# Kernel tuning notes

Hardware: AMD Instinct MI355X
Metric: run time of the kernel (lower is better)

The kernel has to match this reference:

```python
import jax, jax.numpy as jnp
import numpy as np

N, E, IN, H, C = 20000, 320000, 512, 4, 64
HC = H * C
EPS_BN = 1e-5


def setup_inputs() -> dict:
    key = jax.random.key(0)
    ks = jax.random.split(key, 12)
    p = lambda k, shape, s=0.05: jax.random.normal(k, shape, dtype=jnp.float32) * s
    z = lambda n: jnp.zeros((n,), jnp.float32)
    o = lambda n: jnp.ones((n,), jnp.float32)
    return {
        "x": jax.random.normal(ks[0], (N, IN), dtype=jnp.float32),
        "edge_index": jax.random.randint(ks[1], (2, E), 0, N),
        "Wl0": p(ks[2], (IN, HC)), "Wr0": p(ks[3], (IN, HC)),
        "att0": p(ks[4], (H, C)), "b0": z(HC),
        "g0": o(HC), "be0": z(HC), "m0": z(HC), "v0": o(HC),
        "Wl1": p(ks[5], (HC, HC)), "Wr1": p(ks[6], (HC, HC)),
        "att1": p(ks[7], (H, C)), "b1": z(HC),
        "g1": o(HC), "be1": z(HC), "m1": z(HC), "v1": o(HC),
        "Wl2": p(ks[8], (HC, 2)), "Wr2": p(ks[9], (HC, 2)),
        "att2": p(ks[10], (1, 2)), "b2": z(2),
    }


def gatv2_conv(x, Wl, Wr, att, b, ei, concat):
    # GATv2: e_ij = att . LeakyReLU(Wl x_j + Wr x_i); softmax over in-edges of i
    n = x.shape[0]
    h, c = att.shape
    xl = (x @ Wl).reshape(n, h, c)  # source/message transform
    xr = (x @ Wr).reshape(n, h, c)  # target transform
    src, dst = ei[0], ei[1]
    m = xl[src] + xr[dst]                                   # [E,H,C] edge gather
    e = jnp.sum(jax.nn.leaky_relu(m, 0.2) * att, axis=-1)   # [E,H]
    emax = jax.ops.segment_max(e, dst, num_segments=n)      # segment softmax
    emax = jnp.where(jnp.isfinite(emax), emax, 0.0)
    ex = jnp.exp(e - emax[dst])
    denom = jax.ops.segment_sum(ex, dst, num_segments=n)
    alpha = ex / (denom[dst] + 1e-16)                       # [E,H]
    out = jax.ops.segment_sum(alpha[:, :, None] * xl[src], dst, num_segments=n)
    out = out.reshape(n, h * c) if concat else out.mean(axis=1)
    return out + b


def bn_eval(x, g, be, m, v):
    return (x - m) * (g * jax.lax.rsqrt(v + EPS_BN)) + be


def reference(x, edge_index, Wl0, Wr0, att0, b0, g0, be0, m0, v0,
              Wl1, Wr1, att1, b1, g1, be1, m1, v1, Wl2, Wr2, att2, b2):
    loops = jnp.arange(N)
    ei = jnp.concatenate([edge_index, jnp.stack([loops, loops])], axis=1)
    h = gatv2_conv(x, Wl0, Wr0, att0, b0, ei, True)
    h = jax.nn.elu(bn_eval(h, g0, be0, m0, v0))
    h = gatv2_conv(h, Wl1, Wr1, att1, b1, ei, True)
    h = jax.nn.elu(bn_eval(h, g1, be1, m1, v1))
    out = gatv2_conv(h, Wl2, Wr2, att2, b2, ei, False)
    return jax.nn.log_softmax(out, axis=1)
```

## Files before the change

kernel.cpp:

```cpp
#include <hip/hip_runtime.h>
#include <math.h>

#define NN 20000
#define MP 20096
#define EE 320000
#define ET (EE + NN)
#define HC 256
#define EPS_BN 1e-5f

typedef __bf16 bf16x8 __attribute__((ext_vector_type(8)));
typedef float f32x4 __attribute__((ext_vector_type(4)));

__device__ __forceinline__ float4 ld4(const float* p) { return *reinterpret_cast<const float4*>(p); }
__device__ __forceinline__ float lrelu(float x) { return fmaxf(x, 0.f) + 0.2f * fminf(x, 0.f); }

__device__ __forceinline__ unsigned short f2b(float f) {
  unsigned int u = __float_as_uint(f);
  u = (u + 0x7fffu + ((u >> 16) & 1u)) >> 16;
  return (unsigned short)u;
}
__device__ __forceinline__ float b2f(unsigned short u) {
  return __uint_as_float(((unsigned int)u) << 16);
}

__device__ __forceinline__ void gld_lds16(const void* g, void* l) {
  __builtin_amdgcn_global_load_lds(
      (const __attribute__((address_space(1))) unsigned int*)g,
      (__attribute__((address_space(3))) unsigned int*)(unsigned int)(unsigned long long)l,
      16, 0, 0);
}

__global__ __launch_bounds__(256) void convert_x_kernel(const float* __restrict__ x,
                                                        unsigned short* __restrict__ xb) {
  int i = (blockIdx.x * 256 + threadIdx.x) * 4;
  if (i >= NN * 512) return;
  float4 v = ld4(&x[i]);
  ushort4 o;
  o.x = f2b(v.x); o.y = f2b(v.y); o.z = f2b(v.z); o.w = f2b(v.w);
  *reinterpret_cast<ushort4*>(&xb[i]) = o;
}

__global__ __launch_bounds__(256) void convert_w_kernel(const float* __restrict__ Wl,
                                                        const float* __restrict__ Wr,
                                                        unsigned short* __restrict__ Wf,
                                                        int K) {
  int idx = blockIdx.x * 256 + threadIdx.x;
  if (idx >= 512 * K) return;
  int n = idx / K, k = idx - n * K;
  float v = (n < 256) ? Wl[(size_t)k * 256 + n] : Wr[(size_t)k * 256 + (n - 256)];
  Wf[idx] = f2b(v);
}

__global__ __launch_bounds__(256) void gemm_mfma(const unsigned short* __restrict__ A,
                                                 const unsigned short* __restrict__ Bt,
                                                 unsigned short* __restrict__ xlb,
                                                 float* __restrict__ xrf,
                                                 int M, int K) {
  __shared__ unsigned short As[128 * 32];
  __shared__ unsigned short Bs[128 * 32];
  const int wave = threadIdx.x >> 6;
  const int lane = threadIdx.x & 63;
  const int am = lane & 15;
  const int aq = lane >> 4;
  const int wr = (wave >> 1) * 64;
  const int wc = (wave & 1) * 64;
  const int row0 = blockIdx.y * 128;
  const int col0 = blockIdx.x * 128;

  f32x4 acc[4][4] = {};

  for (int kk = 0; kk < K; kk += 32) {
    __syncthreads();
#pragma unroll
    for (int c = 0; c < 2; ++c) {
      int seg = wave * 128 + c * 64 + lane;
      int r = seg >> 2, ks = (seg & 3) * 8;
      gld_lds16(A + (size_t)(row0 + r) * K + kk + ks, &As[(wave * 128 + c * 64) * 8]);
      gld_lds16(Bt + (size_t)(col0 + r) * K + kk + ks, &Bs[(wave * 128 + c * 64) * 8]);
    }
    __syncthreads();

    bf16x8 af[4], bfr[4];
#pragma unroll
    for (int i = 0; i < 4; ++i)
      af[i] = *reinterpret_cast<const bf16x8*>(&As[(wr + i * 16 + am) * 32 + aq * 8]);
#pragma unroll
    for (int j = 0; j < 4; ++j)
      bfr[j] = *reinterpret_cast<const bf16x8*>(&Bs[(wc + j * 16 + am) * 32 + aq * 8]);
#pragma unroll
    for (int i = 0; i < 4; ++i)
#pragma unroll
      for (int j = 0; j < 4; ++j)
        acc[i][j] = __builtin_amdgcn_mfma_f32_16x16x32_bf16(af[i], bfr[j], acc[i][j], 0, 0, 0);
  }

#pragma unroll
  for (int i = 0; i < 4; ++i) {
#pragma unroll
    for (int j = 0; j < 4; ++j) {
      int gcol = col0 + wc + j * 16 + am;
#pragma unroll
      for (int rr = 0; rr < 4; ++rr) {
        int grow = row0 + wr + i * 16 + aq * 4 + rr;
        if (grow < M) {
          float v = acc[i][j][rr];
          if (gcol < 256) xlb[(size_t)grow * 256 + gcol] = f2b(v);
          else            xrf[(size_t)grow * 256 + (gcol - 256)] = v;
        }
      }
    }
  }
}

__global__ __launch_bounds__(256) void hist_kernel(const int* __restrict__ ei,
                                                   int* __restrict__ counts) {
  int e = blockIdx.x * blockDim.x + threadIdx.x;
  if (e >= ET) return;
  int d = (e < EE) ? ei[EE + e] : (e - EE);
  atomicAdd(&counts[d], 1);
}

__global__ __launch_bounds__(1024) void scan_kernel(int* __restrict__ cursor,
                                                    int* __restrict__ offsets) {
  __shared__ int wsum[16];
  const int tid = threadIdx.x;
  const int lane = tid & 63, wv = tid >> 6;
  const int base = tid * 20;
  int vals[20];
  int s = 0;
  if (tid < 1000) {
#pragma unroll
    for (int j = 0; j < 20; ++j) { vals[j] = cursor[base + j]; s += vals[j]; }
  }
  int ssum = s;
#pragma unroll
  for (int off = 1; off < 64; off <<= 1) {
    int t = __shfl_up(ssum, off);
    if (lane >= off) ssum += t;
  }
  if (lane == 63) wsum[wv] = ssum;
  __syncthreads();
  if (wv == 0) {
    int w = (lane < 16) ? wsum[lane] : 0;
#pragma unroll
    for (int off = 1; off < 16; off <<= 1) {
      int t = __shfl_up(w, off);
      if (lane >= off) w += t;
    }
    if (lane < 16) wsum[lane] = w;
  }
  __syncthreads();
  int excl = ssum - s + (wv > 0 ? wsum[wv - 1] : 0);
  if (tid < 1000) {
    int run = excl;
#pragma unroll
    for (int j = 0; j < 20; ++j) { offsets[base + j] = run; cursor[base + j] = run; run += vals[j]; }
  }
  if (tid == 1023) offsets[NN] = wsum[15];
}

__global__ __launch_bounds__(256) void scatter_kernel(const int* __restrict__ ei,
                                                      int* __restrict__ cursor,
                                                      int* __restrict__ srcs) {
  int e = blockIdx.x * blockDim.x + threadIdx.x;
  if (e >= ET) return;
  int s, d;
  if (e < EE) { s = ei[e]; d = ei[EE + e]; } else { s = d = e - EE; }
  int pos = atomicAdd(&cursor[d], 1);
  srcs[pos] = s;
}

__global__ __launch_bounds__(256) void gat_layer(const unsigned short* __restrict__ xlb,
                                                 const float* __restrict__ xrf,
                                                 const float* __restrict__ att,
                                                 const float* __restrict__ bias,
                                                 const float* __restrict__ gam,
                                                 const float* __restrict__ bet,
                                                 const float* __restrict__ mean,
                                                 const float* __restrict__ var,
                                                 const int* __restrict__ offsets,
                                                 const int* __restrict__ srcs,
                                                 unsigned short* __restrict__ hb) {
  const int wave = threadIdx.x >> 6;
  const int lane = threadIdx.x & 63;
  const int node = blockIdx.x * 4 + wave;
  if (node >= NN) return;

  const float4 xr4 = ld4(&xrf[(size_t)node * HC + lane * 4]);
  const float4 a4 = ld4(&att[lane * 4]);
  const int beg = offsets[node];
  const int end = offsets[node + 1];

  float lA = 0.f, lB = 0.f;
  float4 OA = make_float4(0.f, 0.f, 0.f, 0.f);
  float4 OB = make_float4(0.f, 0.f, 0.f, 0.f);

  int i = beg;
  for (; i + 3 < end; i += 4) {
    int s0 = srcs[i], s1 = srcs[i + 1], s2 = srcs[i + 2], s3 = srcs[i + 3];
    ushort4 u0 = *reinterpret_cast<const ushort4*>(&xlb[(size_t)s0 * HC + lane * 4]);
    ushort4 u1 = *reinterpret_cast<const ushort4*>(&xlb[(size_t)s1 * HC + lane * 4]);
    ushort4 u2 = *reinterpret_cast<const ushort4*>(&xlb[(size_t)s2 * HC + lane * 4]);
    ushort4 u3 = *reinterpret_cast<const ushort4*>(&xlb[(size_t)s3 * HC + lane * 4]);
    float4 x0 = make_float4(b2f(u0.x), b2f(u0.y), b2f(u0.z), b2f(u0.w));
    float4 x1 = make_float4(b2f(u1.x), b2f(u1.y), b2f(u1.z), b2f(u1.w));
    float4 x2 = make_float4(b2f(u2.x), b2f(u2.y), b2f(u2.z), b2f(u2.w));
    float4 x3 = make_float4(b2f(u3.x), b2f(u3.y), b2f(u3.z), b2f(u3.w));
    float e0 = lrelu(x0.x + xr4.x) * a4.x + lrelu(x0.y + xr4.y) * a4.y +
               lrelu(x0.z + xr4.z) * a4.z + lrelu(x0.w + xr4.w) * a4.w;
    float e1 = lrelu(x1.x + xr4.x) * a4.x + lrelu(x1.y + xr4.y) * a4.y +
               lrelu(x1.z + xr4.z) * a4.z + lrelu(x1.w + xr4.w) * a4.w;
    float e2 = lrelu(x2.x + xr4.x) * a4.x + lrelu(x2.y + xr4.y) * a4.y +
               lrelu(x2.z + xr4.z) * a4.z + lrelu(x2.w + xr4.w) * a4.w;
    float e3 = lrelu(x3.x + xr4.x) * a4.x + lrelu(x3.y + xr4.y) * a4.y +
               lrelu(x3.z + xr4.z) * a4.z + lrelu(x3.w + xr4.w) * a4.w;
#pragma unroll
    for (int off = 1; off < 16; off <<= 1) {
      e0 += __shfl_xor(e0, off);
      e1 += __shfl_xor(e1, off);
      e2 += __shfl_xor(e2, off);
      e3 += __shfl_xor(e3, off);
    }
    float p0 = __expf(e0), p1 = __expf(e1), p2 = __expf(e2), p3 = __expf(e3);
    lA += p0; lB += p1; lA += p2; lB += p3;
    OA.x += p0 * x0.x; OA.y += p0 * x0.y; OA.z += p0 * x0.z; OA.w += p0 * x0.w;
    OB.x += p1 * x1.x; OB.y += p1 * x1.y; OB.z += p1 * x1.z; OB.w += p1 * x1.w;
    OA.x += p2 * x2.x; OA.y += p2 * x2.y; OA.z += p2 * x2.z; OA.w += p2 * x2.w;
    OB.x += p3 * x3.x; OB.y += p3 * x3.y; OB.z += p3 * x3.z; OB.w += p3 * x3.w;
  }
  for (; i < end; ++i) {
    int s = srcs[i];
    ushort4 u = *reinterpret_cast<const ushort4*>(&xlb[(size_t)s * HC + lane * 4]);
    float4 x0 = make_float4(b2f(u.x), b2f(u.y), b2f(u.z), b2f(u.w));
    float e = lrelu(x0.x + xr4.x) * a4.x + lrelu(x0.y + xr4.y) * a4.y +
              lrelu(x0.z + xr4.z) * a4.z + lrelu(x0.w + xr4.w) * a4.w;
#pragma unroll
    for (int off = 1; off < 16; off <<= 1) e += __shfl_xor(e, off);
    float p = __expf(e);
    lA += p;
    OA.x += p * x0.x; OA.y += p * x0.y; OA.z += p * x0.z; OA.w += p * x0.w;
  }
  float inv = 1.f / (lA + lB);
  float4 O = make_float4(OA.x + OB.x, OA.y + OB.y, OA.z + OB.z, OA.w + OB.w);

  float4 b4 = ld4(&bias[lane * 4]);
  float4 g4 = ld4(&gam[lane * 4]);
  float4 e4 = ld4(&bet[lane * 4]);
  float4 m4 = ld4(&mean[lane * 4]);
  float4 v4 = ld4(&var[lane * 4]);
  float y0 = O.x * inv + b4.x, y1 = O.y * inv + b4.y;
  float y2 = O.z * inv + b4.z, y3 = O.w * inv + b4.w;
  float z0 = (y0 - m4.x) * (g4.x * rsqrtf(v4.x + EPS_BN)) + e4.x;
  float z1 = (y1 - m4.y) * (g4.y * rsqrtf(v4.y + EPS_BN)) + e4.y;
  float z2 = (y2 - m4.z) * (g4.z * rsqrtf(v4.z + EPS_BN)) + e4.z;
  float z3 = (y3 - m4.w) * (g4.w * rsqrtf(v4.w + EPS_BN)) + e4.w;
  ushort4 r;
  r.x = f2b(z0 > 0.f ? z0 : expm1f(z0));
  r.y = f2b(z1 > 0.f ? z1 : expm1f(z1));
  r.z = f2b(z2 > 0.f ? z2 : expm1f(z2));
  r.w = f2b(z3 > 0.f ? z3 : expm1f(z3));
  *reinterpret_cast<ushort4*>(&hb[(size_t)node * HC + lane * 4]) = r;
}

__global__ __launch_bounds__(256) void lin2_kernel(const unsigned short* __restrict__ hb,
                                                   const float* __restrict__ Wl,
                                                   const float* __restrict__ Wr,
                                                   float* __restrict__ xl2,
                                                   float* __restrict__ xr2) {
  const int wave = threadIdx.x >> 6;
  const int lane = threadIdx.x & 63;
  const int node = blockIdx.x * 4 + wave;
  if (node >= NN) return;
  ushort4 h4 = *reinterpret_cast<const ushort4*>(&hb[(size_t)node * HC + lane * 4]);
  float hv[4] = {b2f(h4.x), b2f(h4.y), b2f(h4.z), b2f(h4.w)};
  float l0 = 0.f, l1 = 0.f, r0 = 0.f, r1 = 0.f;
#pragma unroll
  for (int j = 0; j < 4; ++j) {
    int row = lane * 4 + j;
    l0 += hv[j] * Wl[row * 2 + 0];
    l1 += hv[j] * Wl[row * 2 + 1];
    r0 += hv[j] * Wr[row * 2 + 0];
    r1 += hv[j] * Wr[row * 2 + 1];
  }
#pragma unroll
  for (int off = 1; off < 64; off <<= 1) {
    l0 += __shfl_xor(l0, off);
    l1 += __shfl_xor(l1, off);
    r0 += __shfl_xor(r0, off);
    r1 += __shfl_xor(r1, off);
  }
  if (lane == 0) {
    xl2[node * 2 + 0] = l0; xl2[node * 2 + 1] = l1;
    xr2[node * 2 + 0] = r0; xr2[node * 2 + 1] = r1;
  }
}

__global__ __launch_bounds__(256) void gat2_out_kernel(const float* __restrict__ xl2,
                                                       const float* __restrict__ xr2,
                                                       const float* __restrict__ att2,
                                                       const float* __restrict__ b2,
                                                       const int* __restrict__ offsets,
                                                       const int* __restrict__ srcs,
                                                       float* __restrict__ out) {
  const int wave = threadIdx.x >> 6;
  const int lane = threadIdx.x & 63;
  const int node = blockIdx.x * 4 + wave;
  if (node >= NN) return;
  const float a0 = att2[0], a1 = att2[1];
  const float xr0 = xr2[node * 2 + 0], xr1 = xr2[node * 2 + 1];
  const int beg = offsets[node], end = offsets[node + 1];

  float l = 0.f, o0 = 0.f, o1 = 0.f;
  for (int i = beg + lane; i < end; i += 64) {
    int s = srcs[i];
    float x0 = xl2[s * 2 + 0], x1 = xl2[s * 2 + 1];
    float e = lrelu(x0 + xr0) * a0 + lrelu(x1 + xr1) * a1;
    float p = __expf(e);
    l += p;
    o0 += p * x0;
    o1 += p * x1;
  }
#pragma unroll
  for (int off = 1; off < 64; off <<= 1) {
    l += __shfl_xor(l, off);
    o0 += __shfl_xor(o0, off);
    o1 += __shfl_xor(o1, off);
  }
  if (lane == 0) {
    float inv = 1.f / l;
    float t0 = o0 * inv + b2[0];
    float t1 = o1 * inv + b2[1];
    float mx = fmaxf(t0, t1);
    float ls = mx + logf(__expf(t0 - mx) + __expf(t1 - mx));
    out[node * 2 + 0] = t0 - ls;
    out[node * 2 + 1] = t1 - ls;
  }
}

extern "C" void kernel_launch(void* const* d_in, const int* in_sizes, int n_in,
                              void* d_out, int out_size, void* d_ws, size_t ws_size,
                              hipStream_t stream) {
  const float* x    = (const float*)d_in[0];
  const int*   ei   = (const int*)d_in[1];
  const float* Wl0  = (const float*)d_in[2];
  const float* Wr0  = (const float*)d_in[3];
  const float* att0 = (const float*)d_in[4];
  const float* b0   = (const float*)d_in[5];
  const float* g0   = (const float*)d_in[6];
  const float* be0  = (const float*)d_in[7];
  const float* m0   = (const float*)d_in[8];
  const float* v0   = (const float*)d_in[9];
  const float* Wl1  = (const float*)d_in[10];
  const float* Wr1  = (const float*)d_in[11];
  const float* att1 = (const float*)d_in[12];
  const float* b1   = (const float*)d_in[13];
  const float* g1   = (const float*)d_in[14];
  const float* be1  = (const float*)d_in[15];
  const float* m1   = (const float*)d_in[16];
  const float* v1   = (const float*)d_in[17];
  const float* Wl2  = (const float*)d_in[18];
  const float* Wr2  = (const float*)d_in[19];
  const float* att2 = (const float*)d_in[20];
  const float* b2   = (const float*)d_in[21];

  float* xrf = (float*)d_ws;
  unsigned short* xlb = (unsigned short*)(xrf + (size_t)NN * 256);
  unsigned short* hb  = xlb + (size_t)NN * 256;
  unsigned short* xb  = hb + (size_t)MP * 256;
  unsigned short* Wf0 = xb + (size_t)MP * 512;
  unsigned short* Wf1 = Wf0 + 512 * 512;
  float* xl2 = (float*)(Wf1 + 512 * 256);
  float* xr2 = xl2 + 2 * NN;
  int* offsets = (int*)(xr2 + 2 * NN);
  int* cursor  = offsets + (NN + 1);
  int* srcs    = cursor + NN;

  hipMemsetAsync(cursor, 0, NN * sizeof(int), stream);
  hist_kernel<<<(ET + 255) / 256, 256, 0, stream>>>(ei, cursor);
  convert_x_kernel<<<(NN * 512 / 4 + 255) / 256, 256, 0, stream>>>(x, xb);
  convert_w_kernel<<<(512 * 512 + 255) / 256, 256, 0, stream>>>(Wl0, Wr0, Wf0, 512);
  convert_w_kernel<<<(512 * 256 + 255) / 256, 256, 0, stream>>>(Wl1, Wr1, Wf1, 256);
  scan_kernel<<<1, 1024, 0, stream>>>(cursor, offsets);
  scatter_kernel<<<(ET + 255) / 256, 256, 0, stream>>>(ei, cursor, srcs);

  dim3 gemm_grid(4, MP / 128);
  gemm_mfma<<<gemm_grid, 256, 0, stream>>>(xb, Wf0, xlb, xrf, NN, 512);
  gat_layer<<<NN / 4, 256, 0, stream>>>(xlb, xrf, att0, b0, g0, be0, m0, v0, offsets, srcs, hb);
  gemm_mfma<<<gemm_grid, 256, 0, stream>>>(hb, Wf1, xlb, xrf, NN, 256);
  gat_layer<<<NN / 4, 256, 0, stream>>>(xlb, xrf, att1, b1, g1, be1, m1, v1, offsets, srcs, hb);
  lin2_kernel<<<NN / 4, 256, 0, stream>>>(hb, Wl2, Wr2, xl2, xr2);
  gat2_out_kernel<<<NN / 4, 256, 0, stream>>>(xl2, xr2, att2, b2, offsets, srcs, (float*)d_out);
}
```

Baseline: 301.6 us.

## Fuse prep kernels and software-pipeline edge gathers in GAT layer

Merges the x conversion, both weight conversions and the degree histogram into one launch, split by block-index ranges, which removes three kernel launches and lets the pieces overlap. The GAT layer edge loop now loads up to 64 source indices per wave at once, hands them out with shuffles, and keeps three batches of 4-edge feature gathers in flight in a rotating buffer. This is meant to hide gather latency. In exchange it needs more registers and does extra masked work on partial batches.

```diff
diff --git a/kernel.cpp b/kernel.cpp
--- a/kernel.cpp
+++ b/kernel.cpp
@@ -8,6 +8,12 @@
 #define HC 256
 #define EPS_BN 1e-5f
 
+#define PB_CX 5000
+#define PB_W0 1024
+#define PB_W1 512
+#define PB_HIST 1329
+#define PB_TOTAL (PB_CX + PB_W0 + PB_W1 + PB_HIST)
+
 typedef __bf16 bf16x8 __attribute__((ext_vector_type(8)));
 typedef float f32x4 __attribute__((ext_vector_type(4)));
 
@@ -30,25 +36,44 @@
       16, 0, 0);
 }
 
-__global__ __launch_bounds__(256) void convert_x_kernel(const float* __restrict__ x,
-                                                        unsigned short* __restrict__ xb) {
-  int i = (blockIdx.x * 256 + threadIdx.x) * 4;
-  if (i >= NN * 512) return;
-  float4 v = ld4(&x[i]);
-  ushort4 o;
-  o.x = f2b(v.x); o.y = f2b(v.y); o.z = f2b(v.z); o.w = f2b(v.w);
-  *reinterpret_cast<ushort4*>(&xb[i]) = o;
-}
-
-__global__ __launch_bounds__(256) void convert_w_kernel(const float* __restrict__ Wl,
-                                                        const float* __restrict__ Wr,
-                                                        unsigned short* __restrict__ Wf,
-                                                        int K) {
-  int idx = blockIdx.x * 256 + threadIdx.x;
-  if (idx >= 512 * K) return;
-  int n = idx / K, k = idx - n * K;
-  float v = (n < 256) ? Wl[(size_t)k * 256 + n] : Wr[(size_t)k * 256 + (n - 256)];
-  Wf[idx] = f2b(v);
+__global__ __launch_bounds__(256) void prep_kernel(const float* __restrict__ x,
+                                                   unsigned short* __restrict__ xb,
+                                                   const float* __restrict__ Wl0,
+                                                   const float* __restrict__ Wr0,
+                                                   unsigned short* __restrict__ Wf0,
+                                                   const float* __restrict__ Wl1,
+                                                   const float* __restrict__ Wr1,
+                                                   unsigned short* __restrict__ Wf1,
+                                                   const int* __restrict__ ei,
+                                                   int* __restrict__ counts) {
+  const int b = blockIdx.x;
+  const int tid = threadIdx.x;
+  if (b < PB_CX) {
+    int i = (b * 256 + tid) * 8;
+    float4 v0 = ld4(&x[i]);
+    float4 v1 = ld4(&x[i + 4]);
+    ushort4 o0, o1;
+    o0.x = f2b(v0.x); o0.y = f2b(v0.y); o0.z = f2b(v0.z); o0.w = f2b(v0.w);
+    o1.x = f2b(v1.x); o1.y = f2b(v1.y); o1.z = f2b(v1.z); o1.w = f2b(v1.w);
+    *reinterpret_cast<ushort4*>(&xb[i]) = o0;
+    *reinterpret_cast<ushort4*>(&xb[i + 4]) = o1;
+  } else if (b < PB_CX + PB_W0) {
+    int idx = (b - PB_CX) * 256 + tid;
+    int n = idx >> 9, k = idx & 511;
+    float v = (n < 256) ? Wl0[(size_t)k * 256 + n] : Wr0[(size_t)k * 256 + (n - 256)];
+    Wf0[idx] = f2b(v);
+  } else if (b < PB_CX + PB_W0 + PB_W1) {
+    int idx = (b - PB_CX - PB_W0) * 256 + tid;
+    int n = idx >> 8, k = idx & 255;
+    float v = (n < 256) ? Wl1[(size_t)k * 256 + n] : Wr1[(size_t)k * 256 + (n - 256)];
+    Wf1[idx] = f2b(v);
+  } else {
+    int e = (b - PB_CX - PB_W0 - PB_W1) * 256 + tid;
+    if (e < ET) {
+      int d = (e < EE) ? ei[EE + e] : (e - EE);
+      atomicAdd(&counts[d], 1);
+    }
+  }
 }
 
 __global__ __launch_bounds__(256) void gemm_mfma(const unsigned short* __restrict__ A,
@@ -112,14 +137,6 @@
   }
 }
 
-__global__ __launch_bounds__(256) void hist_kernel(const int* __restrict__ ei,
-                                                   int* __restrict__ counts) {
-  int e = blockIdx.x * blockDim.x + threadIdx.x;
-  if (e >= ET) return;
-  int d = (e < EE) ? ei[EE + e] : (e - EE);
-  atomicAdd(&counts[d], 1);
-}
-
 __global__ __launch_bounds__(1024) void scan_kernel(int* __restrict__ cursor,
                                                     int* __restrict__ offsets) {
   __shared__ int wsum[16];
@@ -189,57 +206,76 @@
   const float4 xr4 = ld4(&xrf[(size_t)node * HC + lane * 4]);
   const float4 a4 = ld4(&att[lane * 4]);
   const int beg = offsets[node];
-  const int end = offsets[node + 1];
+  const int deg = offsets[node + 1] - beg;
 
   float lA = 0.f, lB = 0.f;
   float4 OA = make_float4(0.f, 0.f, 0.f, 0.f);
   float4 OB = make_float4(0.f, 0.f, 0.f, 0.f);
 
-  int i = beg;
-  for (; i + 3 < end; i += 4) {
-    int s0 = srcs[i], s1 = srcs[i + 1], s2 = srcs[i + 2], s3 = srcs[i + 3];
-    ushort4 u0 = *reinterpret_cast<const ushort4*>(&xlb[(size_t)s0 * HC + lane * 4]);
-    ushort4 u1 = *reinterpret_cast<const ushort4*>(&xlb[(size_t)s1 * HC + lane * 4]);
-    ushort4 u2 = *reinterpret_cast<const ushort4*>(&xlb[(size_t)s2 * HC + lane * 4]);
-    ushort4 u3 = *reinterpret_cast<const ushort4*>(&xlb[(size_t)s3 * HC + lane * 4]);
-    float4 x0 = make_float4(b2f(u0.x), b2f(u0.y), b2f(u0.z), b2f(u0.w));
-    float4 x1 = make_float4(b2f(u1.x), b2f(u1.y), b2f(u1.z), b2f(u1.w));
-    float4 x2 = make_float4(b2f(u2.x), b2f(u2.y), b2f(u2.z), b2f(u2.w));
-    float4 x3 = make_float4(b2f(u3.x), b2f(u3.y), b2f(u3.z), b2f(u3.w));
-    float e0 = lrelu(x0.x + xr4.x) * a4.x + lrelu(x0.y + xr4.y) * a4.y +
-               lrelu(x0.z + xr4.z) * a4.z + lrelu(x0.w + xr4.w) * a4.w;
-    float e1 = lrelu(x1.x + xr4.x) * a4.x + lrelu(x1.y + xr4.y) * a4.y +
-               lrelu(x1.z + xr4.z) * a4.z + lrelu(x1.w + xr4.w) * a4.w;
-    float e2 = lrelu(x2.x + xr4.x) * a4.x + lrelu(x2.y + xr4.y) * a4.y +
-               lrelu(x2.z + xr4.z) * a4.z + lrelu(x2.w + xr4.w) * a4.w;
-    float e3 = lrelu(x3.x + xr4.x) * a4.x + lrelu(x3.y + xr4.y) * a4.y +
-               lrelu(x3.z + xr4.z) * a4.z + lrelu(x3.w + xr4.w) * a4.w;
-#pragma unroll
-    for (int off = 1; off < 16; off <<= 1) {
-      e0 += __shfl_xor(e0, off);
-      e1 += __shfl_xor(e1, off);
-      e2 += __shfl_xor(e2, off);
-      e3 += __shfl_xor(e3, off);
-    }
-    float p0 = __expf(e0), p1 = __expf(e1), p2 = __expf(e2), p3 = __expf(e3);
-    lA += p0; lB += p1; lA += p2; lB += p3;
-    OA.x += p0 * x0.x; OA.y += p0 * x0.y; OA.z += p0 * x0.z; OA.w += p0 * x0.w;
-    OB.x += p1 * x1.x; OB.y += p1 * x1.y; OB.z += p1 * x1.z; OB.w += p1 * x1.w;
-    OA.x += p2 * x2.x; OA.y += p2 * x2.y; OA.z += p2 * x2.z; OA.w += p2 * x2.w;
-    OB.x += p3 * x3.x; OB.y += p3 * x3.y; OB.z += p3 * x3.z; OB.w += p3 * x3.w;
-  }
-  for (; i < end; ++i) {
-    int s = srcs[i];
-    ushort4 u = *reinterpret_cast<const ushort4*>(&xlb[(size_t)s * HC + lane * 4]);
-    float4 x0 = make_float4(b2f(u.x), b2f(u.y), b2f(u.z), b2f(u.w));
-    float e = lrelu(x0.x + xr4.x) * a4.x + lrelu(x0.y + xr4.y) * a4.y +
-              lrelu(x0.z + xr4.z) * a4.z + lrelu(x0.w + xr4.w) * a4.w;
-#pragma unroll
-    for (int off = 1; off < 16; off <<= 1) e += __shfl_xor(e, off);
-    float p = __expf(e);
-    lA += p;
-    OA.x += p * x0.x; OA.y += p * x0.y; OA.z += p * x0.z; OA.w += p * x0.w;
-  }
+  for (int base = 0; base < deg; base += 64) {
+    const int chunk = min(64, deg - base);
+    const int s_reg = srcs[beg + base + min(lane, chunk - 1)];
+    const int nb = (chunk + 3) >> 2;
+
+    ushort4 buf0[4], buf1[4], buf2[4];
+
+#define ISSUE(r, buf)                                                              \
+    {                                                                              \
+      _Pragma("unroll")                                                            \
+      for (int j = 0; j < 4; ++j) {                                                \
+        int idx = (r) * 4 + j;                                                     \
+        int sv = __shfl(s_reg, idx < chunk ? idx : 0);                             \
+        buf[j] = *reinterpret_cast<const ushort4*>(&xlb[(size_t)sv * HC + lane * 4]); \
+      }                                                                            \
+    }
+
+#define COMPUTE(r, buf)                                                            \
+    {                                                                              \
+      float e[4], xv[4][4];                                                        \
+      _Pragma("unroll")                                                            \
+      for (int j = 0; j < 4; ++j) {                                                \
+        xv[j][0] = b2f(buf[j].x); xv[j][1] = b2f(buf[j].y);                        \
+        xv[j][2] = b2f(buf[j].z); xv[j][3] = b2f(buf[j].w);                        \
+        e[j] = lrelu(xv[j][0] + xr4.x) * a4.x + lrelu(xv[j][1] + xr4.y) * a4.y +   \
+               lrelu(xv[j][2] + xr4.z) * a4.z + lrelu(xv[j][3] + xr4.w) * a4.w;    \
+      }                                                                            \
+      _Pragma("unroll")                                                            \
+      for (int off = 1; off < 16; off <<= 1) {                                     \
+        e[0] += __shfl_xor(e[0], off); e[1] += __shfl_xor(e[1], off);              \
+        e[2] += __shfl_xor(e[2], off); e[3] += __shfl_xor(e[3], off);              \
+      }                                                                            \
+      float p0 = __expf(e[0]), p1 = __expf(e[1]);                                  \
+      float p2 = __expf(e[2]), p3 = __expf(e[3]);                                  \
+      if ((r) * 4 + 0 >= chunk) p0 = 0.f;                                          \
+      if ((r) * 4 + 1 >= chunk) p1 = 0.f;                                          \
+      if ((r) * 4 + 2 >= chunk) p2 = 0.f;                                          \
+      if ((r) * 4 + 3 >= chunk) p3 = 0.f;                                          \
+      lA += p0; lB += p1; lA += p2; lB += p3;                                      \
+      OA.x += p0 * xv[0][0]; OA.y += p0 * xv[0][1];                                \
+      OA.z += p0 * xv[0][2]; OA.w += p0 * xv[0][3];                                \
+      OB.x += p1 * xv[1][0]; OB.y += p1 * xv[1][1];                                \
+      OB.z += p1 * xv[1][2]; OB.w += p1 * xv[1][3];                                \
+      OA.x += p2 * xv[2][0]; OA.y += p2 * xv[2][1];                                \
+      OA.z += p2 * xv[2][2]; OA.w += p2 * xv[2][3];                                \
+      OB.x += p3 * xv[3][0]; OB.y += p3 * xv[3][1];                                \
+      OB.z += p3 * xv[3][2]; OB.w += p3 * xv[3][3];                                \
+    }
+
+    ISSUE(0, buf0);
+    ISSUE(1, buf1);
+    ISSUE(2, buf2);
+    int r = 0;
+    while (r < nb) {
+      COMPUTE(r, buf0); if (r + 3 < nb) ISSUE(r + 3, buf0); ++r;
+      if (r >= nb) break;
+      COMPUTE(r, buf1); if (r + 3 < nb) ISSUE(r + 3, buf1); ++r;
+      if (r >= nb) break;
+      COMPUTE(r, buf2); if (r + 3 < nb) ISSUE(r + 3, buf2); ++r;
+    }
+#undef ISSUE
+#undef COMPUTE
+  }
+
   float inv = 1.f / (lA + lB);
   float4 O = make_float4(OA.x + OB.x, OA.y + OB.y, OA.z + OB.z, OA.w + OB.w);
 
@@ -254,12 +290,12 @@
   float z1 = (y1 - m4.y) * (g4.y * rsqrtf(v4.y + EPS_BN)) + e4.y;
   float z2 = (y2 - m4.z) * (g4.z * rsqrtf(v4.z + EPS_BN)) + e4.z;
   float z3 = (y3 - m4.w) * (g4.w * rsqrtf(v4.w + EPS_BN)) + e4.w;
-  ushort4 r;
-  r.x = f2b(z0 > 0.f ? z0 : expm1f(z0));
-  r.y = f2b(z1 > 0.f ? z1 : expm1f(z1));
-  r.z = f2b(z2 > 0.f ? z2 : expm1f(z2));
-  r.w = f2b(z3 > 0.f ? z3 : expm1f(z3));
-  *reinterpret_cast<ushort4*>(&hb[(size_t)node * HC + lane * 4]) = r;
+  ushort4 r4o;
+  r4o.x = f2b(z0 > 0.f ? z0 : expm1f(z0));
+  r4o.y = f2b(z1 > 0.f ? z1 : expm1f(z1));
+  r4o.z = f2b(z2 > 0.f ? z2 : expm1f(z2));
+  r4o.w = f2b(z3 > 0.f ? z3 : expm1f(z3));
+  *reinterpret_cast<ushort4*>(&hb[(size_t)node * HC + lane * 4]) = r4o;
 }
 
 __global__ __launch_bounds__(256) void lin2_kernel(const unsigned short* __restrict__ hb,
@@ -376,10 +412,7 @@
   int* srcs    = cursor + NN;
 
   hipMemsetAsync(cursor, 0, NN * sizeof(int), stream);
-  hist_kernel<<<(ET + 255) / 256, 256, 0, stream>>>(ei, cursor);
-  convert_x_kernel<<<(NN * 512 / 4 + 255) / 256, 256, 0, stream>>>(x, xb);
-  convert_w_kernel<<<(512 * 512 + 255) / 256, 256, 0, stream>>>(Wl0, Wr0, Wf0, 512);
-  convert_w_kernel<<<(512 * 256 + 255) / 256, 256, 0, stream>>>(Wl1, Wr1, Wf1, 256);
+  prep_kernel<<<PB_TOTAL, 256, 0, stream>>>(x, xb, Wl0, Wr0, Wf0, Wl1, Wr1, Wf1, ei, cursor);
   scan_kernel<<<1, 1024, 0, stream>>>(cursor, offsets);
   scatter_kernel<<<(ET + 255) / 256, 256, 0, stream>>>(ei, cursor, srcs);
 
```

Measured after the change: 310.4 us. +2.9%, slower.

## Fuse all stages into one persistent kernel with atomic grid barriers

Applied to the files above, without the earlier changes.

Replaces the chain of about a dozen kernel launches with a single persistent kernel of 512 blocks. The stages are separated by software grid barriers built from an atomic counter with sleep-spin. Layer-1 output is fused directly into the final linear projection, which drops the hb write and the separate lin2 pass. This targets launch overhead and inter-kernel gaps, but the GEMM now loops tiles over fewer blocks, the scan runs on a single block, and co-residency of all 512 blocks is assumed.

```diff
diff --git a/kernel.cpp b/kernel.cpp
--- a/kernel.cpp
+++ b/kernel.cpp
@@ -8,6 +8,11 @@
 #define HC 256
 #define EPS_BN 1e-5f
 
+#define GRID_B 512
+#define NTHREADS (GRID_B * 256)
+#define NWAVES (GRID_B * 4)
+#define GEMM_TILES 628
+
 typedef __bf16 bf16x8 __attribute__((ext_vector_type(8)));
 typedef float f32x4 __attribute__((ext_vector_type(4)));
 
@@ -30,42 +35,42 @@
       16, 0, 0);
 }
 
-__global__ __launch_bounds__(256) void convert_x_kernel(const float* __restrict__ x,
-                                                        unsigned short* __restrict__ xb) {
-  int i = (blockIdx.x * 256 + threadIdx.x) * 4;
-  if (i >= NN * 512) return;
-  float4 v = ld4(&x[i]);
-  ushort4 o;
-  o.x = f2b(v.x); o.y = f2b(v.y); o.z = f2b(v.z); o.w = f2b(v.w);
-  *reinterpret_cast<ushort4*>(&xb[i]) = o;
-}
-
-__global__ __launch_bounds__(256) void convert_w_kernel(const float* __restrict__ Wl,
-                                                        const float* __restrict__ Wr,
-                                                        unsigned short* __restrict__ Wf,
-                                                        int K) {
-  int idx = blockIdx.x * 256 + threadIdx.x;
-  if (idx >= 512 * K) return;
-  int n = idx / K, k = idx - n * K;
-  float v = (n < 256) ? Wl[(size_t)k * 256 + n] : Wr[(size_t)k * 256 + (n - 256)];
-  Wf[idx] = f2b(v);
-}
-
-__global__ __launch_bounds__(256) void gemm_mfma(const unsigned short* __restrict__ A,
-                                                 const unsigned short* __restrict__ Bt,
-                                                 unsigned short* __restrict__ xlb,
-                                                 float* __restrict__ xrf,
-                                                 int M, int K) {
-  __shared__ unsigned short As[128 * 32];
-  __shared__ unsigned short Bs[128 * 32];
-  const int wave = threadIdx.x >> 6;
-  const int lane = threadIdx.x & 63;
+__device__ __forceinline__ void gbar(int* cnt, int target) {
+  __threadfence();
+  __syncthreads();
+  if (threadIdx.x == 0) {
+    atomicAdd(cnt, 1);
+    while (atomicAdd(cnt, 0) < target) __builtin_amdgcn_s_sleep(8);
+  }
+  __syncthreads();
+  __threadfence();
+}
+
+struct KParams {
+  const float* x; const int* ei;
+  const float *Wl0, *Wr0, *att0, *b0, *g0, *be0, *m0, *v0;
+  const float *Wl1, *Wr1, *att1, *b1, *g1, *be1, *m1, *v1;
+  const float *Wl2, *Wr2, *att2, *b2;
+  unsigned short *xb, *Wf0, *Wf1, *xlb, *hb;
+  float *xrf, *xl2, *xr2;
+  int *offsets, *cursor, *srcs, *bar;
+  float* out;
+};
+
+__device__ __forceinline__ void gemm_tile(const unsigned short* __restrict__ A,
+                                          const unsigned short* __restrict__ Bt,
+                                          unsigned short* __restrict__ xlb,
+                                          float* __restrict__ xrf,
+                                          int K, int t, int tid,
+                                          unsigned short* As, unsigned short* Bs) {
+  const int wave = tid >> 6;
+  const int lane = tid & 63;
   const int am = lane & 15;
   const int aq = lane >> 4;
   const int wr = (wave >> 1) * 64;
   const int wc = (wave & 1) * 64;
-  const int row0 = blockIdx.y * 128;
-  const int col0 = blockIdx.x * 128;
+  const int row0 = (t >> 2) * 128;
+  const int col0 = (t & 3) * 128;
 
   f32x4 acc[4][4] = {};
 
@@ -102,7 +107,7 @@
 #pragma unroll
       for (int rr = 0; rr < 4; ++rr) {
         int grow = row0 + wr + i * 16 + aq * 4 + rr;
-        if (grow < M) {
+        if (grow < NN) {
           float v = acc[i][j][rr];
           if (gcol < 256) xlb[(size_t)grow * 256 + gcol] = f2b(v);
           else            xrf[(size_t)grow * 256 + (gcol - 256)] = v;
@@ -112,85 +117,14 @@
   }
 }
 
-__global__ __launch_bounds__(256) void hist_kernel(const int* __restrict__ ei,
-                                                   int* __restrict__ counts) {
-  int e = blockIdx.x * blockDim.x + threadIdx.x;
-  if (e >= ET) return;
-  int d = (e < EE) ? ei[EE + e] : (e - EE);
-  atomicAdd(&counts[d], 1);
-}
-
-__global__ __launch_bounds__(1024) void scan_kernel(int* __restrict__ cursor,
-                                                    int* __restrict__ offsets) {
-  __shared__ int wsum[16];
-  const int tid = threadIdx.x;
-  const int lane = tid & 63, wv = tid >> 6;
-  const int base = tid * 20;
-  int vals[20];
-  int s = 0;
-  if (tid < 1000) {
-#pragma unroll
-    for (int j = 0; j < 20; ++j) { vals[j] = cursor[base + j]; s += vals[j]; }
-  }
-  int ssum = s;
-#pragma unroll
-  for (int off = 1; off < 64; off <<= 1) {
-    int t = __shfl_up(ssum, off);
-    if (lane >= off) ssum += t;
-  }
-  if (lane == 63) wsum[wv] = ssum;
-  __syncthreads();
-  if (wv == 0) {
-    int w = (lane < 16) ? wsum[lane] : 0;
-#pragma unroll
-    for (int off = 1; off < 16; off <<= 1) {
-      int t = __shfl_up(w, off);
-      if (lane >= off) w += t;
-    }
-    if (lane < 16) wsum[lane] = w;
-  }
-  __syncthreads();
-  int excl = ssum - s + (wv > 0 ? wsum[wv - 1] : 0);
-  if (tid < 1000) {
-    int run = excl;
-#pragma unroll
-    for (int j = 0; j < 20; ++j) { offsets[base + j] = run; cursor[base + j] = run; run += vals[j]; }
-  }
-  if (tid == 1023) offsets[NN] = wsum[15];
-}
-
-__global__ __launch_bounds__(256) void scatter_kernel(const int* __restrict__ ei,
-                                                      int* __restrict__ cursor,
-                                                      int* __restrict__ srcs) {
-  int e = blockIdx.x * blockDim.x + threadIdx.x;
-  if (e >= ET) return;
-  int s, d;
-  if (e < EE) { s = ei[e]; d = ei[EE + e]; } else { s = d = e - EE; }
-  int pos = atomicAdd(&cursor[d], 1);
-  srcs[pos] = s;
-}
-
-__global__ __launch_bounds__(256) void gat_layer(const unsigned short* __restrict__ xlb,
-                                                 const float* __restrict__ xrf,
-                                                 const float* __restrict__ att,
-                                                 const float* __restrict__ bias,
-                                                 const float* __restrict__ gam,
-                                                 const float* __restrict__ bet,
-                                                 const float* __restrict__ mean,
-                                                 const float* __restrict__ var,
-                                                 const int* __restrict__ offsets,
-                                                 const int* __restrict__ srcs,
-                                                 unsigned short* __restrict__ hb) {
-  const int wave = threadIdx.x >> 6;
-  const int lane = threadIdx.x & 63;
-  const int node = blockIdx.x * 4 + wave;
-  if (node >= NN) return;
-
+__device__ __forceinline__ void gat_node(const unsigned short* __restrict__ xlb,
+                                         const float* __restrict__ xrf,
+                                         const int* __restrict__ srcs,
+                                         int beg, int end, int node, int lane,
+                                         float4 a4, float4 b4, float4 g4, float4 e4,
+                                         float4 m4, float4 v4,
+                                         float& z0, float& z1, float& z2, float& z3) {
   const float4 xr4 = ld4(&xrf[(size_t)node * HC + lane * 4]);
-  const float4 a4 = ld4(&att[lane * 4]);
-  const int beg = offsets[node];
-  const int end = offsets[node + 1];
-
   float lA = 0.f, lB = 0.f;
   float4 OA = make_float4(0.f, 0.f, 0.f, 0.f);
   float4 OB = make_float4(0.f, 0.f, 0.f, 0.f);
@@ -241,127 +175,224 @@
     OA.x += p * x0.x; OA.y += p * x0.y; OA.z += p * x0.z; OA.w += p * x0.w;
   }
   float inv = 1.f / (lA + lB);
-  float4 O = make_float4(OA.x + OB.x, OA.y + OB.y, OA.z + OB.z, OA.w + OB.w);
-
-  float4 b4 = ld4(&bias[lane * 4]);
-  float4 g4 = ld4(&gam[lane * 4]);
-  float4 e4 = ld4(&bet[lane * 4]);
-  float4 m4 = ld4(&mean[lane * 4]);
-  float4 v4 = ld4(&var[lane * 4]);
-  float y0 = O.x * inv + b4.x, y1 = O.y * inv + b4.y;
-  float y2 = O.z * inv + b4.z, y3 = O.w * inv + b4.w;
-  float z0 = (y0 - m4.x) * (g4.x * rsqrtf(v4.x + EPS_BN)) + e4.x;
-  float z1 = (y1 - m4.y) * (g4.y * rsqrtf(v4.y + EPS_BN)) + e4.y;
-  float z2 = (y2 - m4.z) * (g4.z * rsqrtf(v4.z + EPS_BN)) + e4.z;
-  float z3 = (y3 - m4.w) * (g4.w * rsqrtf(v4.w + EPS_BN)) + e4.w;
-  ushort4 r;
-  r.x = f2b(z0 > 0.f ? z0 : expm1f(z0));
-  r.y = f2b(z1 > 0.f ? z1 : expm1f(z1));
-  r.z = f2b(z2 > 0.f ? z2 : expm1f(z2));
-  r.w = f2b(z3 > 0.f ? z3 : expm1f(z3));
-  *reinterpret_cast<ushort4*>(&hb[(size_t)node * HC + lane * 4]) = r;
-}
-
-__global__ __launch_bounds__(256) void lin2_kernel(const unsigned short* __restrict__ hb,
-                                                   const float* __restrict__ Wl,
-                                                   const float* __restrict__ Wr,
-                                                   float* __restrict__ xl2,
-                                                   float* __restrict__ xr2) {
-  const int wave = threadIdx.x >> 6;
-  const int lane = threadIdx.x & 63;
-  const int node = blockIdx.x * 4 + wave;
-  if (node >= NN) return;
-  ushort4 h4 = *reinterpret_cast<const ushort4*>(&hb[(size_t)node * HC + lane * 4]);
-  float hv[4] = {b2f(h4.x), b2f(h4.y), b2f(h4.z), b2f(h4.w)};
-  float l0 = 0.f, l1 = 0.f, r0 = 0.f, r1 = 0.f;
-#pragma unroll
-  for (int j = 0; j < 4; ++j) {
-    int row = lane * 4 + j;
-    l0 += hv[j] * Wl[row * 2 + 0];
-    l1 += hv[j] * Wl[row * 2 + 1];
-    r0 += hv[j] * Wr[row * 2 + 0];
-    r1 += hv[j] * Wr[row * 2 + 1];
-  }
-#pragma unroll
-  for (int off = 1; off < 64; off <<= 1) {
-    l0 += __shfl_xor(l0, off);
-    l1 += __shfl_xor(l1, off);
-    r0 += __shfl_xor(r0, off);
-    r1 += __shfl_xor(r1, off);
-  }
-  if (lane == 0) {
-    xl2[node * 2 + 0] = l0; xl2[node * 2 + 1] = l1;
-    xr2[node * 2 + 0] = r0; xr2[node * 2 + 1] = r1;
-  }
-}
-
-__global__ __launch_bounds__(256) void gat2_out_kernel(const float* __restrict__ xl2,
-                                                       const float* __restrict__ xr2,
-                                                       const float* __restrict__ att2,
-                                                       const float* __restrict__ b2,
-                                                       const int* __restrict__ offsets,
-                                                       const int* __restrict__ srcs,
-                                                       float* __restrict__ out) {
-  const int wave = threadIdx.x >> 6;
-  const int lane = threadIdx.x & 63;
-  const int node = blockIdx.x * 4 + wave;
-  if (node >= NN) return;
-  const float a0 = att2[0], a1 = att2[1];
-  const float xr0 = xr2[node * 2 + 0], xr1 = xr2[node * 2 + 1];
-  const int beg = offsets[node], end = offsets[node + 1];
-
-  float l = 0.f, o0 = 0.f, o1 = 0.f;
-  for (int i = beg + lane; i < end; i += 64) {
-    int s = srcs[i];
-    float x0 = xl2[s * 2 + 0], x1 = xl2[s * 2 + 1];
-    float e = lrelu(x0 + xr0) * a0 + lrelu(x1 + xr1) * a1;
-    float p = __expf(e);
-    l += p;
-    o0 += p * x0;
-    o1 += p * x1;
-  }
-#pragma unroll
-  for (int off = 1; off < 64; off <<= 1) {
-    l += __shfl_xor(l, off);
-    o0 += __shfl_xor(o0, off);
-    o1 += __shfl_xor(o1, off);
-  }
-  if (lane == 0) {
-    float inv = 1.f / l;
-    float t0 = o0 * inv + b2[0];
-    float t1 = o1 * inv + b2[1];
-    float mx = fmaxf(t0, t1);
-    float ls = mx + logf(__expf(t0 - mx) + __expf(t1 - mx));
-    out[node * 2 + 0] = t0 - ls;
-    out[node * 2 + 1] = t1 - ls;
+  float y0 = (OA.x + OB.x) * inv + b4.x, y1 = (OA.y + OB.y) * inv + b4.y;
+  float y2 = (OA.z + OB.z) * inv + b4.z, y3 = (OA.w + OB.w) * inv + b4.w;
+  z0 = (y0 - m4.x) * (g4.x * rsqrtf(v4.x + EPS_BN)) + e4.x;
+  z1 = (y1 - m4.y) * (g4.y * rsqrtf(v4.y + EPS_BN)) + e4.y;
+  z2 = (y2 - m4.z) * (g4.z * rsqrtf(v4.z + EPS_BN)) + e4.z;
+  z3 = (y3 - m4.w) * (g4.w * rsqrtf(v4.w + EPS_BN)) + e4.w;
+  z0 = (z0 > 0.f) ? z0 : expm1f(z0);
+  z1 = (z1 > 0.f) ? z1 : expm1f(z1);
+  z2 = (z2 > 0.f) ? z2 : expm1f(z2);
+  z3 = (z3 > 0.f) ? z3 : expm1f(z3);
+}
+
+__global__ __launch_bounds__(256, 2) void mega_kernel(KParams P) {
+  __shared__ unsigned short As[128 * 32];
+  __shared__ unsigned short Bs[128 * 32];
+  __shared__ int wsum[4];
+
+  const int b = blockIdx.x;
+  const int tid = threadIdx.x;
+  const int gtid = b * 256 + tid;
+  const int lane = tid & 63;
+  const int w = (b << 2) | (tid >> 6);
+
+  for (int i = gtid; i < NN * 512 / 8; i += NTHREADS) {
+    int base = i * 8;
+    float4 v0 = ld4(&P.x[base]);
+    float4 v1 = ld4(&P.x[base + 4]);
+    ushort4 o0, o1;
+    o0.x = f2b(v0.x); o0.y = f2b(v0.y); o0.z = f2b(v0.z); o0.w = f2b(v0.w);
+    o1.x = f2b(v1.x); o1.y = f2b(v1.y); o1.z = f2b(v1.z); o1.w = f2b(v1.w);
+    *reinterpret_cast<ushort4*>(&P.xb[base]) = o0;
+    *reinterpret_cast<ushort4*>(&P.xb[base + 4]) = o1;
+  }
+  for (int i = gtid; i < 512 * 512; i += NTHREADS) {
+    int n = i >> 9, k = i & 511;
+    float v = (n < 256) ? P.Wl0[(size_t)k * 256 + n] : P.Wr0[(size_t)k * 256 + (n - 256)];
+    P.Wf0[i] = f2b(v);
+  }
+  for (int i = gtid; i < 512 * 256; i += NTHREADS) {
+    int n = i >> 8, k = i & 255;
+    float v = (n < 256) ? P.Wl1[(size_t)k * 256 + n] : P.Wr1[(size_t)k * 256 + (n - 256)];
+    P.Wf1[i] = f2b(v);
+  }
+  for (int e = gtid; e < ET; e += NTHREADS) {
+    int d = (e < EE) ? P.ei[EE + e] : (e - EE);
+    atomicAdd(&P.cursor[d], 1);
+  }
+  gbar(P.bar, 1 * GRID_B);
+
+  if (b == 0) {
+    const int wv = tid >> 6;
+    const int base = tid * 79;
+    int s = 0;
+    for (int j = 0; j < 79; ++j) {
+      int idx = base + j;
+      if (idx < NN) s += P.cursor[idx];
+    }
+    int inc = s;
+#pragma unroll
+    for (int off = 1; off < 64; off <<= 1) {
+      int t = __shfl_up(inc, off);
+      if (lane >= off) inc += t;
+    }
+    if (lane == 63) wsum[wv] = inc;
+    __syncthreads();
+    if (tid == 0) {
+      int run = 0;
+      for (int i2 = 0; i2 < 4; ++i2) { int t = wsum[i2]; wsum[i2] = run; run += t; }
+      P.offsets[NN] = run;
+    }
+    __syncthreads();
+    int run = inc - s + wsum[wv];
+    for (int j = 0; j < 79; ++j) {
+      int idx = base + j;
+      if (idx < NN) {
+        int v = P.cursor[idx];
+        P.offsets[idx] = run;
+        P.cursor[idx] = run;
+        run += v;
+      }
+    }
+  }
+  gbar(P.bar, 2 * GRID_B);
+
+  for (int e = gtid; e < ET; e += NTHREADS) {
+    int s, d;
+    if (e < EE) { s = P.ei[e]; d = P.ei[EE + e]; } else { s = d = e - EE; }
+    int pos = atomicAdd(&P.cursor[d], 1);
+    P.srcs[pos] = s;
+  }
+  gbar(P.bar, 3 * GRID_B);
+
+  for (int t = b; t < GEMM_TILES; t += GRID_B)
+    gemm_tile(P.xb, P.Wf0, P.xlb, P.xrf, 512, t, tid, As, Bs);
+  gbar(P.bar, 4 * GRID_B);
+
+  {
+    const float4 a4 = ld4(&P.att0[lane * 4]);
+    const float4 b4 = ld4(&P.b0[lane * 4]);
+    const float4 g4 = ld4(&P.g0[lane * 4]);
+    const float4 e4 = ld4(&P.be0[lane * 4]);
+    const float4 m4 = ld4(&P.m0[lane * 4]);
+    const float4 v4 = ld4(&P.v0[lane * 4]);
+    for (int node = w; node < NN; node += NWAVES) {
+      float z0, z1, z2, z3;
+      gat_node(P.xlb, P.xrf, P.srcs, P.offsets[node], P.offsets[node + 1], node, lane,
+               a4, b4, g4, e4, m4, v4, z0, z1, z2, z3);
+      ushort4 r;
+      r.x = f2b(z0); r.y = f2b(z1); r.z = f2b(z2); r.w = f2b(z3);
+      *reinterpret_cast<ushort4*>(&P.hb[(size_t)node * HC + lane * 4]) = r;
+    }
+  }
+  gbar(P.bar, 5 * GRID_B);
+
+  for (int t = b; t < GEMM_TILES; t += GRID_B)
+    gemm_tile(P.hb, P.Wf1, P.xlb, P.xrf, 256, t, tid, As, Bs);
+  gbar(P.bar, 6 * GRID_B);
+
+  {
+    const float4 a4 = ld4(&P.att1[lane * 4]);
+    const float4 b4 = ld4(&P.b1[lane * 4]);
+    const float4 g4 = ld4(&P.g1[lane * 4]);
+    const float4 e4 = ld4(&P.be1[lane * 4]);
+    const float4 m4 = ld4(&P.m1[lane * 4]);
+    const float4 v4 = ld4(&P.v1[lane * 4]);
+    const int row = lane * 4;
+    const float wl00 = P.Wl2[(row + 0) * 2], wl01 = P.Wl2[(row + 0) * 2 + 1];
+    const float wl10 = P.Wl2[(row + 1) * 2], wl11 = P.Wl2[(row + 1) * 2 + 1];
+    const float wl20 = P.Wl2[(row + 2) * 2], wl21 = P.Wl2[(row + 2) * 2 + 1];
+    const float wl30 = P.Wl2[(row + 3) * 2], wl31 = P.Wl2[(row + 3) * 2 + 1];
+    const float wr00 = P.Wr2[(row + 0) * 2], wr01 = P.Wr2[(row + 0) * 2 + 1];
+    const float wr10 = P.Wr2[(row + 1) * 2], wr11 = P.Wr2[(row + 1) * 2 + 1];
+    const float wr20 = P.Wr2[(row + 2) * 2], wr21 = P.Wr2[(row + 2) * 2 + 1];
+    const float wr30 = P.Wr2[(row + 3) * 2], wr31 = P.Wr2[(row + 3) * 2 + 1];
+    for (int node = w; node < NN; node += NWAVES) {
+      float z0, z1, z2, z3;
+      gat_node(P.xlb, P.xrf, P.srcs, P.offsets[node], P.offsets[node + 1], node, lane,
+               a4, b4, g4, e4, m4, v4, z0, z1, z2, z3);
+      float pl0 = z0 * wl00 + z1 * wl10 + z2 * wl20 + z3 * wl30;
+      float pl1 = z0 * wl01 + z1 * wl11 + z2 * wl21 + z3 * wl31;
+      float pr0 = z0 * wr00 + z1 * wr10 + z2 * wr20 + z3 * wr30;
+      float pr1 = z0 * wr01 + z1 * wr11 + z2 * wr21 + z3 * wr31;
+#pragma unroll
+      for (int off = 1; off < 64; off <<= 1) {
+        pl0 += __shfl_xor(pl0, off);
+        pl1 += __shfl_xor(pl1, off);
+        pr0 += __shfl_xor(pr0, off);
+        pr1 += __shfl_xor(pr1, off);
+      }
+      if (lane == 0) {
+        P.xl2[node * 2 + 0] = pl0; P.xl2[node * 2 + 1] = pl1;
+        P.xr2[node * 2 + 0] = pr0; P.xr2[node * 2 + 1] = pr1;
+      }
+    }
+  }
+  gbar(P.bar, 7 * GRID_B);
+
+  {
+    const float a0 = P.att2[0], a1 = P.att2[1];
+    const float bb0 = P.b2[0], bb1 = P.b2[1];
+    for (int node = w; node < NN; node += NWAVES) {
+      const float xr0 = P.xr2[node * 2 + 0], xr1 = P.xr2[node * 2 + 1];
+      const int beg = P.offsets[node], end = P.offsets[node + 1];
+      float l = 0.f, o0 = 0.f, o1 = 0.f;
+      for (int i = beg + lane; i < end; i += 64) {
+        int s = P.srcs[i];
+        float x0 = P.xl2[s * 2 + 0], x1 = P.xl2[s * 2 + 1];
+        float e = lrelu(x0 + xr0) * a0 + lrelu(x1 + xr1) * a1;
+        float p = __expf(e);
+        l += p;
+        o0 += p * x0;
+        o1 += p * x1;
+      }
+#pragma unroll
+      for (int off = 1; off < 64; off <<= 1) {
+        l += __shfl_xor(l, off);
+        o0 += __shfl_xor(o0, off);
+        o1 += __shfl_xor(o1, off);
+      }
+      if (lane == 0) {
+        float inv = 1.f / l;
+        float t0 = o0 * inv + bb0;
+        float t1 = o1 * inv + bb1;
+        float mx = fmaxf(t0, t1);
+        float ls = mx + logf(__expf(t0 - mx) + __expf(t1 - mx));
+        P.out[node * 2 + 0] = t0 - ls;
+        P.out[node * 2 + 1] = t1 - ls;
+      }
+    }
   }
 }
 
 extern "C" void kernel_launch(void* const* d_in, const int* in_sizes, int n_in,
                               void* d_out, int out_size, void* d_ws, size_t ws_size,
                               hipStream_t stream) {
-  const float* x    = (const float*)d_in[0];
-  const int*   ei   = (const int*)d_in[1];
-  const float* Wl0  = (const float*)d_in[2];
-  const float* Wr0  = (const float*)d_in[3];
-  const float* att0 = (const float*)d_in[4];
-  const float* b0   = (const float*)d_in[5];
-  const float* g0   = (const float*)d_in[6];
-  const float* be0  = (const float*)d_in[7];
-  const float* m0   = (const float*)d_in[8];
-  const float* v0   = (const float*)d_in[9];
-  const float* Wl1  = (const float*)d_in[10];
-  const float* Wr1  = (const float*)d_in[11];
-  const float* att1 = (const float*)d_in[12];
-  const float* b1   = (const float*)d_in[13];
-  const float* g1   = (const float*)d_in[14];
-  const float* be1  = (const float*)d_in[15];
-  const float* m1   = (const float*)d_in[16];
-  const float* v1   = (const float*)d_in[17];
-  const float* Wl2  = (const float*)d_in[18];
-  const float* Wr2  = (const float*)d_in[19];
-  const float* att2 = (const float*)d_in[20];
-  const float* b2   = (const float*)d_in[21];
+  KParams P;
+  P.x    = (const float*)d_in[0];
+  P.ei   = (const int*)d_in[1];
+  P.Wl0  = (const float*)d_in[2];
+  P.Wr0  = (const float*)d_in[3];
+  P.att0 = (const float*)d_in[4];
+  P.b0   = (const float*)d_in[5];
+  P.g0   = (const float*)d_in[6];
+  P.be0  = (const float*)d_in[7];
+  P.m0   = (const float*)d_in[8];
+  P.v0   = (const float*)d_in[9];
+  P.Wl1  = (const float*)d_in[10];
+  P.Wr1  = (const float*)d_in[11];
+  P.att1 = (const float*)d_in[12];
+  P.b1   = (const float*)d_in[13];
+  P.g1   = (const float*)d_in[14];
+  P.be1  = (const float*)d_in[15];
+  P.m1   = (const float*)d_in[16];
+  P.v1   = (const float*)d_in[17];
+  P.Wl2  = (const float*)d_in[18];
+  P.Wr2  = (const float*)d_in[19];
+  P.att2 = (const float*)d_in[20];
+  P.b2   = (const float*)d_in[21];
 
   float* xrf = (float*)d_ws;
   unsigned short* xlb = (unsigned short*)(xrf + (size_t)NN * 256);
@@ -373,21 +404,15 @@
   float* xr2 = xl2 + 2 * NN;
   int* offsets = (int*)(xr2 + 2 * NN);
   int* cursor  = offsets + (NN + 1);
-  int* srcs    = cursor + NN;
-
-  hipMemsetAsync(cursor, 0, NN * sizeof(int), stream);
-  hist_kernel<<<(ET + 255) / 256, 256, 0, stream>>>(ei, cursor);
-  convert_x_kernel<<<(NN * 512 / 4 + 255) / 256, 256, 0, stream>>>(x, xb);
-  convert_w_kernel<<<(512 * 512 + 255) / 256, 256, 0, stream>>>(Wl0, Wr0, Wf0, 512);
-  convert_w_kernel<<<(512 * 256 + 255) / 256, 256, 0, stream>>>(Wl1, Wr1, Wf1, 256);
-  scan_kernel<<<1, 1024, 0, stream>>>(cursor, offsets);
-  scatter_kernel<<<(ET + 255) / 256, 256, 0, stream>>>(ei, cursor, srcs);
-
-  dim3 gemm_grid(4, MP / 128);
-  gemm_mfma<<<gemm_grid, 256, 0, stream>>>(xb, Wf0, xlb, xrf, NN, 512);
-  gat_layer<<<NN / 4, 256, 0, stream>>>(xlb, xrf, att0, b0, g0, be0, m0, v0, offsets, srcs, hb);
-  gemm_mfma<<<gemm_grid, 256, 0, stream>>>(hb, Wf1, xlb, xrf, NN, 256);
-  gat_layer<<<NN / 4, 256, 0, stream>>>(xlb, xrf, att1, b1, g1, be1, m1, v1, offsets, srcs, hb);
-  lin2_kernel<<<NN / 4, 256, 0, stream>>>(hb, Wl2, Wr2, xl2, xr2);
-  gat2_out_kernel<<<NN / 4, 256, 0, stream>>>(xl2, xr2, att2, b2, offsets, srcs, (float*)d_out);
-}
+  int* bar     = cursor + NN;
+  int* srcs    = bar + 1;
+
+  P.xrf = xrf; P.xlb = xlb; P.hb = hb; P.xb = xb;
+  P.Wf0 = Wf0; P.Wf1 = Wf1;
+  P.xl2 = xl2; P.xr2 = xr2;
+  P.offsets = offsets; P.cursor = cursor; P.srcs = srcs; P.bar = bar;
+  P.out = (float*)d_out;
+
+  hipMemsetAsync(cursor, 0, (NN + 1) * sizeof(int), stream);
+  mega_kernel<<<GRID_B, 256, 0, stream>>>(P);
+}
```

After: 1.117 ms. 3.7x slower.
